# Optimization experiments

Hardware: AMD Instinct MI355X
Metric: run time of the kernel (lower is better)

The kernel has to match this reference:

```python
import jax, jax.numpy as jnp
import numpy as np

B, N, H, HEADS = 8, 1024, 512, 4  # batch graphs, nodes/graph, graph_hsz, attention heads
R = 64  # relations per graph (passthrough)


def setup_inputs() -> dict:
    key = jax.random.key(0)
    k1, k2, k3, k4, k5, k6, k7 = jax.random.split(key, 7)
    adjs = jax.random.randint(k1, (B, N, N), 0, 2, dtype=jnp.int32)  # 0 => masked
    nodes = jax.random.normal(k2, (B, N, H), dtype=jnp.float32)
    triples = jax.random.normal(k3, (B, R, H), dtype=jnp.float32)   # unused in gat path
    relations = jax.random.normal(k4, (B, R, H), dtype=jnp.float32)  # passthrough
    node_num = jnp.full((B,), N, dtype=jnp.int32)  # all graphs full => no padding branch
    s = 1.0 / np.sqrt(H)
    Wq = (jax.random.normal(k5, (H, H), dtype=jnp.float32) * s)
    Wk = (jax.random.normal(k6, (H, H), dtype=jnp.float32) * s)
    Wv = (jax.random.normal(k7, (H, H), dtype=jnp.float32) * s)
    return {"adjs": adjs, "triples": triples, "nodes": nodes, "node_num": node_num,
            "relations": relations, "Wq": Wq, "Wk": Wk, "Wv": Wv}


def reference(adjs, triples, nodes, node_num, relations, Wq, Wk, Wv):
    b, n, h = nodes.shape
    dk = h // HEADS
    scale = 1.0 / jnp.sqrt(jnp.float32(h))  # torch divides by sqrt(key_dim)=sqrt(H)

    def to_heads(x, W):  # [B,N,H] -> [B,heads,N,dk]; matches split(dim=-1)+stack
        return (x @ W).reshape(b, n, HEADS, dk).transpose(0, 2, 1, 3)

    Q = to_heads(nodes, Wq)
    K = to_heads(nodes, Wk)
    V = to_heads(nodes, Wv)
    att = jnp.einsum('bhnd,bhmd->bhnm', Q, K) * scale
    att = jnp.where((adjs == 0)[:, None, :, :], -jnp.inf, att)
    p = jax.nn.softmax(att, axis=-1)  # dropout_p = blockdrop = 0.0 => identity
    out = jnp.einsum('bhnm,bhmd->bhnd', p, V)
    out = out.transpose(0, 2, 1, 3).reshape(b, n, h)  # concat heads along feature dim
    out = jax.nn.relu(out)
    return (out, relations)
```

## Files before the change

### kernel.cpp

```cpp
#include <hip/hip_runtime.h>
#include <stdint.h>

typedef __attribute__((ext_vector_type(4))) float f32x4;
typedef __attribute__((ext_vector_type(8))) short bf16x8;
typedef unsigned long long ull;

#define GLB_AS const __attribute__((address_space(1)))
#define LDS_AS __attribute__((address_space(3)))

__device__ __forceinline__ short f2bf(float f) {
    union { float f; unsigned u; } x; x.f = f;
    unsigned r = x.u + 0x7FFFu + ((x.u >> 16) & 1u);
    return (short)(r >> 16);
}

__global__ void k_cvt_nodes(const float* __restrict__ in, short* __restrict__ out, int n) {
    int i = (blockIdx.x * 256 + threadIdx.x) * 8;
    if (i + 8 > n) return;
    float4 a = *(const float4*)(in + i);
    float4 b = *(const float4*)(in + i + 4);
    bf16x8 v;
    v[0] = f2bf(a.x); v[1] = f2bf(a.y); v[2] = f2bf(a.z); v[3] = f2bf(a.w);
    v[4] = f2bf(b.x); v[5] = f2bf(b.y); v[6] = f2bf(b.z); v[7] = f2bf(b.w);
    *(bf16x8*)(out + i) = v;
}

__global__ void k_cvt_wT(const float* __restrict__ Wq, const float* __restrict__ Wk,
                         const float* __restrict__ Wv, short* __restrict__ WT) {
    int g = blockIdx.x * 256 + threadIdx.x;
    int j = g >> 9;
    int k = g & 511;
    int w = j >> 9;
    int n = j & 511;
    const float* W = (w == 0) ? Wq : (w == 1) ? Wk : Wv;
    WT[g] = f2bf(W[k * 512 + n]);
}

__global__ void k_pack_adj(const int* __restrict__ adjs, unsigned* __restrict__ packed) {
    int g = blockIdx.x * 256 + threadIdx.x;
    int wv = g >> 6, lane = g & 63;
    ull m = __ballot(adjs[(size_t)wv * 64 + lane] != 0);
    if (lane == 0) *(ull*)(packed + (size_t)wv * 2) = m;
}

__global__ __launch_bounds__(256) void k_gemm_qkv(const short* __restrict__ A,
                                                  const short* __restrict__ WT,
                                                  short* __restrict__ C) {
    __shared__ short Asm[2][128 * 32];
    __shared__ short Bsm[2][128 * 32];
    const int tid = threadIdx.x;
    const int l = tid & 63, w = tid >> 6;
    const int wr = w >> 1, wc = w & 1;
    const int c16 = l & 15, g = l >> 4;
    const int row0 = blockIdx.x * 128, n0 = blockIdx.y * 128;
    f32x4 acc[4][4] = {};

    auto stage = [&](int kt, int bsel) {
        const int k0 = kt * 32;
#pragma unroll
        for (int i = 0; i < 2; ++i) {
            int ch = tid + 256 * i;
            int r = ch >> 2, gc = ch & 3;
            __builtin_amdgcn_global_load_lds((GLB_AS unsigned*)(A + (row0 + r) * 512 + k0 + 8 * gc),
                                             (LDS_AS unsigned*)(&Asm[bsel][ch * 8]), 16, 0, 0);
            __builtin_amdgcn_global_load_lds((GLB_AS unsigned*)(WT + (n0 + r) * 512 + k0 + 8 * gc),
                                             (LDS_AS unsigned*)(&Bsm[bsel][ch * 8]), 16, 0, 0);
        }
    };

    stage(0, 0);
    asm volatile("s_waitcnt vmcnt(0)" ::: "memory");
    __syncthreads();

    for (int kt = 0; kt < 16; ++kt) {
        const int cur = kt & 1;
        if (kt < 15) stage(kt + 1, cur ^ 1);
        bf16x8 af[4], bfr[4];
#pragma unroll
        for (int mf = 0; mf < 4; ++mf)
            af[mf] = *(const bf16x8*)&Asm[cur][(wr * 64 + mf * 16 + c16) * 32 + 8 * g];
#pragma unroll
        for (int nf = 0; nf < 4; ++nf)
            bfr[nf] = *(const bf16x8*)&Bsm[cur][(wc * 64 + nf * 16 + c16) * 32 + 8 * g];
#pragma unroll
        for (int mf = 0; mf < 4; ++mf)
#pragma unroll
            for (int nf = 0; nf < 4; ++nf)
                acc[mf][nf] = __builtin_amdgcn_mfma_f32_16x16x32_bf16(af[mf], bfr[nf], acc[mf][nf], 0, 0, 0);
        asm volatile("s_waitcnt vmcnt(0)" ::: "memory");
        __syncthreads();
    }
#pragma unroll
    for (int mf = 0; mf < 4; ++mf)
#pragma unroll
        for (int nf = 0; nf < 4; ++nf)
#pragma unroll
            for (int r = 0; r < 4; ++r) {
                int row = row0 + wr * 64 + mf * 16 + 4 * g + r;
                int col = n0 + wc * 64 + nf * 16 + c16;
                C[row * 1536 + col] = f2bf(acc[mf][nf][r]);
            }
}

__global__ __launch_bounds__(256) void k_transpose_v(const short* __restrict__ QKV, short* __restrict__ Vt) {
    __shared__ short tile[64 * 65];
    const int b = blockIdx.x, n0 = blockIdx.y * 64, d0 = blockIdx.z * 64;
    const int t = threadIdx.x;
#pragma unroll
    for (int i = 0; i < 16; ++i) {
        int idx = t + 256 * i;
        int nn = idx >> 6, dd = idx & 63;
        tile[nn * 65 + dd] = QKV[(b * 1024 + n0 + nn) * 1536 + 1024 + d0 + dd];
    }
    __syncthreads();
#pragma unroll
    for (int i = 0; i < 16; ++i) {
        int idx = t + 256 * i;
        int dd = idx >> 6, nn = idx & 63;
        Vt[(b * 512 + d0 + dd) * 1024 + n0 + nn] = tile[nn * 65 + dd];
    }
}

__global__ __launch_bounds__(256) void k_attn(const short* __restrict__ QKV, const short* __restrict__ Vt,
                                              const unsigned* __restrict__ packed, float* __restrict__ out) {
    __shared__ short Ksm[2][64 * 128];
    __shared__ short Vsm[2][128 * 64];
    __shared__ short Psm[64 * 72];
    const int bh = blockIdx.x;
    const int b = bh >> 2, h = bh & 3;
    const int q0 = blockIdx.y * 64;
    const int tid = threadIdx.x, l = tid & 63, w = tid >> 6;
    const int c16 = l & 15, g = l >> 4;
    const int qw = q0 + w * 16;
    const float scale = 0.044194173824159216f;

    bf16x8 aq[4];
    const short* Qrow = QKV + (size_t)(b * 1024 + qw + c16) * 1536 + h * 128;
#pragma unroll
    for (int kf = 0; kf < 4; ++kf)
        aq[kf] = *(const bf16x8*)(Qrow + kf * 32 + 8 * g);

    f32x4 acc_o[8] = {};
    float l_lane[4] = {0.f, 0.f, 0.f, 0.f};

    const short* Kbase = QKV + (size_t)(b * 1024) * 1536 + 512 + h * 128;
    const short* Vtbase = Vt + (size_t)(b * 512 + h * 128) * 1024;
    const ull* adjp = (const ull*)packed + (size_t)(b * 1024 + qw + 4 * g) * 16;

    auto stage = [&](int t, int bsel) {
        const int m0 = t * 64;
#pragma unroll
        for (int i = 0; i < 4; ++i) {
            int ch = tid + 256 * i;
            int mr = ch >> 4, gc = ch & 15;
            int gs = gc ^ (mr & 7);
            __builtin_amdgcn_global_load_lds((GLB_AS unsigned*)(Kbase + (size_t)(m0 + mr) * 1536 + 8 * gs),
                                             (LDS_AS unsigned*)(&Ksm[bsel][ch * 8]), 16, 0, 0);
        }
#pragma unroll
        for (int i = 0; i < 4; ++i) {
            int ch = tid + 256 * i;
            int dr = ch >> 3, gc = ch & 7;
            int gs = gc ^ (dr & 7);
            __builtin_amdgcn_global_load_lds((GLB_AS unsigned*)(Vtbase + (size_t)dr * 1024 + m0 + 8 * gs),
                                             (LDS_AS unsigned*)(&Vsm[bsel][ch * 8]), 16, 0, 0);
        }
    };

    ull mcur[4], mnxt[4] = {0, 0, 0, 0};
    stage(0, 0);
#pragma unroll
    for (int r = 0; r < 4; ++r) mcur[r] = adjp[r * 16];
    asm volatile("s_waitcnt vmcnt(0)" ::: "memory");
    __syncthreads();

    for (int t = 0; t < 16; ++t) {
        const int cur = t & 1;
        if (t < 15) {
            stage(t + 1, cur ^ 1);
#pragma unroll
            for (int r = 0; r < 4; ++r) mnxt[r] = adjp[r * 16 + t + 1];
        }

        f32x4 s[4] = {};
#pragma unroll
        for (int nf = 0; nf < 4; ++nf) {
            const int mrow = nf * 16 + c16;
#pragma unroll
            for (int kf = 0; kf < 4; ++kf) {
                int chunk = (kf * 4 + g) ^ (mrow & 7);
                bf16x8 bk = *(const bf16x8*)&Ksm[cur][mrow * 128 + chunk * 8];
                s[nf] = __builtin_amdgcn_mfma_f32_16x16x32_bf16(aq[kf], bk, s[nf], 0, 0, 0);
            }
        }
#pragma unroll
        for (int r = 0; r < 4; ++r) {
            unsigned mlo = (unsigned)mcur[r];
            unsigned mhi = (unsigned)(mcur[r] >> 32);
#pragma unroll
            for (int nf = 0; nf < 4; ++nf) {
                unsigned hw = (nf < 2) ? mlo : mhi;
                unsigned bit = (hw >> ((nf & 1) * 16 + c16)) & 1u;
                float e = __expf(s[nf][r] * scale);
                float pv = bit ? e : 0.f;
                l_lane[r] += pv;
                Psm[(w * 16 + 4 * g + r) * 72 + nf * 16 + c16] = f2bf(pv);
            }
        }
#pragma unroll
        for (int ks = 0; ks < 2; ++ks) {
            bf16x8 ap = *(const bf16x8*)&Psm[(w * 16 + c16) * 72 + ks * 32 + 8 * g];
#pragma unroll
            for (int df = 0; df < 8; ++df) {
                const int drow = df * 16 + c16;
                int chunk = (ks * 4 + g) ^ (drow & 7);
                bf16x8 bv = *(const bf16x8*)&Vsm[cur][drow * 64 + chunk * 8];
                acc_o[df] = __builtin_amdgcn_mfma_f32_16x16x32_bf16(ap, bv, acc_o[df], 0, 0, 0);
            }
        }
        asm volatile("s_waitcnt vmcnt(0)" ::: "memory");
        __syncthreads();
#pragma unroll
        for (int r = 0; r < 4; ++r) mcur[r] = mnxt[r];
    }
    float inv_l[4];
#pragma unroll
    for (int r = 0; r < 4; ++r) {
        float ls = l_lane[r];
        ls += __shfl_xor(ls, 1);
        ls += __shfl_xor(ls, 2);
        ls += __shfl_xor(ls, 4);
        ls += __shfl_xor(ls, 8);
        inv_l[r] = 1.f / ls;
    }
#pragma unroll
    for (int df = 0; df < 8; ++df)
#pragma unroll
        for (int r = 0; r < 4; ++r) {
            int q = qw + 4 * g + r;
            float o = fmaxf(acc_o[df][r] * inv_l[r], 0.f);
            out[(size_t)(b * 1024 + q) * 512 + h * 128 + df * 16 + c16] = o;
        }
}

__global__ void k_copy_rel(const float* __restrict__ in, float* __restrict__ out, int n) {
    int i = (blockIdx.x * 256 + threadIdx.x) * 4;
    if (i + 4 > n) return;
    *(float4*)(out + i) = *(const float4*)(in + i);
}

extern "C" void kernel_launch(void* const* d_in, const int* in_sizes, int n_in,
                              void* d_out, int out_size, void* d_ws, size_t ws_size,
                              hipStream_t stream) {
    const int*   adjs      = (const int*)d_in[0];
    const float* nodes     = (const float*)d_in[2];
    const float* relations = (const float*)d_in[4];
    const float* Wq        = (const float*)d_in[5];
    const float* Wk        = (const float*)d_in[6];
    const float* Wv        = (const float*)d_in[7];

    char* ws = (char*)d_ws;
    short* nodes_bf   = (short*)(ws);
    short* WT         = (short*)(ws + 8388608);
    short* QKV        = (short*)(ws + 9961472);
    short* Vt         = (short*)(ws + 35127296);
    unsigned* adjpack = (unsigned*)(ws + 43515904);

    float* out     = (float*)d_out;
    float* out_rel = out + 4194304;

    k_cvt_nodes<<<dim3(2048), dim3(256), 0, stream>>>(nodes, nodes_bf, 4194304);
    k_cvt_wT<<<dim3(3072), dim3(256), 0, stream>>>(Wq, Wk, Wv, WT);
    k_pack_adj<<<dim3(32768), dim3(256), 0, stream>>>(adjs, adjpack);
    k_gemm_qkv<<<dim3(64, 12), dim3(256), 0, stream>>>(nodes_bf, WT, QKV);
    k_transpose_v<<<dim3(8, 16, 8), dim3(256), 0, stream>>>(QKV, Vt);
    k_attn<<<dim3(32, 16), dim3(256), 0, stream>>>(QKV, Vt, adjpack, out);
    k_copy_rel<<<dim3(256), dim3(256), 0, stream>>>(relations, out_rel, 262144);
}
```

Measured before the change: 91.63 us.

## Merge preprocessing kernels, swizzle GEMM tiles, and restructure attention softmax pipeline

Folds the three preprocessing kernels into one launch and the relation copy into the V-transpose launch, cutting the launch count from seven to four. Remaps GEMM workgroups with an XCD-aware swizzle to improve cache locality. In attention, computes S transposed so each lane holds four consecutive key columns. It uses exp2 with a prescaled constant, packed bf16 conversion and per-wave P buffers. It also replaces full syncthreads with partial vmcnt waits plus raw barriers and sets wave priority around the MFMA blocks. The finer-grained waits risk ordering bugs if the vmcnt counts are wrong.

```diff
diff --git a/kernel.cpp b/kernel.cpp
--- a/kernel.cpp
+++ b/kernel.cpp
@@ -14,33 +14,31 @@
     return (short)(r >> 16);
 }
 
-__global__ void k_cvt_nodes(const float* __restrict__ in, short* __restrict__ out, int n) {
-    int i = (blockIdx.x * 256 + threadIdx.x) * 8;
-    if (i + 8 > n) return;
-    float4 a = *(const float4*)(in + i);
-    float4 b = *(const float4*)(in + i + 4);
-    bf16x8 v;
-    v[0] = f2bf(a.x); v[1] = f2bf(a.y); v[2] = f2bf(a.z); v[3] = f2bf(a.w);
-    v[4] = f2bf(b.x); v[5] = f2bf(b.y); v[6] = f2bf(b.z); v[7] = f2bf(b.w);
-    *(bf16x8*)(out + i) = v;
-}
-
-__global__ void k_cvt_wT(const float* __restrict__ Wq, const float* __restrict__ Wk,
-                         const float* __restrict__ Wv, short* __restrict__ WT) {
-    int g = blockIdx.x * 256 + threadIdx.x;
-    int j = g >> 9;
-    int k = g & 511;
-    int w = j >> 9;
-    int n = j & 511;
-    const float* W = (w == 0) ? Wq : (w == 1) ? Wk : Wv;
-    WT[g] = f2bf(W[k * 512 + n]);
-}
-
-__global__ void k_pack_adj(const int* __restrict__ adjs, unsigned* __restrict__ packed) {
-    int g = blockIdx.x * 256 + threadIdx.x;
-    int wv = g >> 6, lane = g & 63;
-    ull m = __ballot(adjs[(size_t)wv * 64 + lane] != 0);
-    if (lane == 0) *(ull*)(packed + (size_t)wv * 2) = m;
+__global__ void k_pre(const float* __restrict__ nodes, short* __restrict__ nodes_bf,
+                      const float* __restrict__ Wq, const float* __restrict__ Wk,
+                      const float* __restrict__ Wv, short* __restrict__ WT,
+                      const int* __restrict__ adjs, unsigned* __restrict__ packed) {
+    int bi = blockIdx.x, tid = threadIdx.x;
+    if (bi < 2048) {
+        int i = (bi * 256 + tid) * 8;
+        float4 a = *(const float4*)(nodes + i);
+        float4 b = *(const float4*)(nodes + i + 4);
+        bf16x8 v;
+        v[0] = f2bf(a.x); v[1] = f2bf(a.y); v[2] = f2bf(a.z); v[3] = f2bf(a.w);
+        v[4] = f2bf(b.x); v[5] = f2bf(b.y); v[6] = f2bf(b.z); v[7] = f2bf(b.w);
+        *(bf16x8*)(nodes_bf + i) = v;
+    } else if (bi < 5120) {
+        int g = (bi - 2048) * 256 + tid;
+        int j = g >> 9, k = g & 511;
+        int w = j >> 9, n = j & 511;
+        const float* W = (w == 0) ? Wq : (w == 1) ? Wk : Wv;
+        WT[g] = f2bf(W[k * 512 + n]);
+    } else {
+        int g = (bi - 5120) * 256 + tid;
+        int wv = g >> 6, lane = g & 63;
+        ull m = __ballot(adjs[(size_t)wv * 64 + lane] != 0);
+        if (lane == 0) *(ull*)(packed + (size_t)wv * 2) = m;
+    }
 }
 
 __global__ __launch_bounds__(256) void k_gemm_qkv(const short* __restrict__ A,
@@ -52,7 +50,9 @@
     const int l = tid & 63, w = tid >> 6;
     const int wr = w >> 1, wc = w & 1;
     const int c16 = l & 15, g = l >> 4;
-    const int row0 = blockIdx.x * 128, n0 = blockIdx.y * 128;
+    const int wg = blockIdx.x;
+    const int swz = (wg & 7) * 96 + (wg >> 3);
+    const int row0 = (swz / 12) * 128, n0 = (swz % 12) * 128;
     f32x4 acc[4][4] = {};
 
     auto stage = [&](int kt, int bsel) {
@@ -102,10 +102,16 @@
             }
 }
 
-__global__ __launch_bounds__(256) void k_transpose_v(const short* __restrict__ QKV, short* __restrict__ Vt) {
+__global__ __launch_bounds__(256) void k_mid(const short* __restrict__ QKV, short* __restrict__ Vt,
+                                             const float* __restrict__ rel_in, float* __restrict__ rel_out) {
     __shared__ short tile[64 * 65];
-    const int b = blockIdx.x, n0 = blockIdx.y * 64, d0 = blockIdx.z * 64;
-    const int t = threadIdx.x;
+    const int bi = blockIdx.x, t = threadIdx.x;
+    if (bi >= 1024) {
+        int i = ((bi - 1024) * 256 + t) * 4;
+        *(float4*)(rel_out + i) = *(const float4*)(rel_in + i);
+        return;
+    }
+    const int b = bi >> 7, n0 = ((bi >> 3) & 15) * 64, d0 = (bi & 7) * 64;
 #pragma unroll
     for (int i = 0; i < 16; ++i) {
         int idx = t + 256 * i;
@@ -125,14 +131,14 @@
                                               const unsigned* __restrict__ packed, float* __restrict__ out) {
     __shared__ short Ksm[2][64 * 128];
     __shared__ short Vsm[2][128 * 64];
-    __shared__ short Psm[64 * 72];
+    __shared__ short Psm[4][16 * 68];
     const int bh = blockIdx.x;
     const int b = bh >> 2, h = bh & 3;
     const int q0 = blockIdx.y * 64;
-    const int tid = threadIdx.x, l = tid & 63, w = tid >> 6;
+    const int tid = threadIdx.x, l = tid & 63, wid = tid >> 6;
     const int c16 = l & 15, g = l >> 4;
-    const int qw = q0 + w * 16;
-    const float scale = 0.044194173824159216f;
+    const int qw = q0 + wid * 16;
+    const float kscale = 0.06375872022286384f;
 
     bf16x8 aq[4];
     const short* Qrow = QKV + (size_t)(b * 1024 + qw + c16) * 1536 + h * 128;
@@ -141,11 +147,11 @@
         aq[kf] = *(const bf16x8*)(Qrow + kf * 32 + 8 * g);
 
     f32x4 acc_o[8] = {};
-    float l_lane[4] = {0.f, 0.f, 0.f, 0.f};
+    float l_lane = 0.f;
 
     const short* Kbase = QKV + (size_t)(b * 1024) * 1536 + 512 + h * 128;
     const short* Vtbase = Vt + (size_t)(b * 512 + h * 128) * 1024;
-    const ull* adjp = (const ull*)packed + (size_t)(b * 1024 + qw + 4 * g) * 16;
+    const ull* adjq = (const ull*)packed + (size_t)(b * 1024 + qw + c16) * 16;
 
     auto stage = [&](int t, int bsel) {
         const int m0 = t * 64;
@@ -167,72 +173,85 @@
         }
     };
 
-    ull mcur[4], mnxt[4] = {0, 0, 0, 0};
+    ull mcur, mnxt = 0;
+    mcur = adjq[0];
     stage(0, 0);
-#pragma unroll
-    for (int r = 0; r < 4; ++r) mcur[r] = adjp[r * 16];
     asm volatile("s_waitcnt vmcnt(0)" ::: "memory");
-    __syncthreads();
+    __builtin_amdgcn_s_barrier();
 
     for (int t = 0; t < 16; ++t) {
         const int cur = t & 1;
         if (t < 15) {
+            mnxt = adjq[t + 1];
             stage(t + 1, cur ^ 1);
-#pragma unroll
-            for (int r = 0; r < 4; ++r) mnxt[r] = adjp[r * 16 + t + 1];
         }
 
         f32x4 s[4] = {};
+        __builtin_amdgcn_s_setprio(1);
 #pragma unroll
         for (int nf = 0; nf < 4; ++nf) {
             const int mrow = nf * 16 + c16;
 #pragma unroll
             for (int kf = 0; kf < 4; ++kf) {
                 int chunk = (kf * 4 + g) ^ (mrow & 7);
-                bf16x8 bk = *(const bf16x8*)&Ksm[cur][mrow * 128 + chunk * 8];
-                s[nf] = __builtin_amdgcn_mfma_f32_16x16x32_bf16(aq[kf], bk, s[nf], 0, 0, 0);
+                bf16x8 ak = *(const bf16x8*)&Ksm[cur][mrow * 128 + chunk * 8];
+                s[nf] = __builtin_amdgcn_mfma_f32_16x16x32_bf16(ak, aq[kf], s[nf], 0, 0, 0);
             }
         }
-#pragma unroll
-        for (int r = 0; r < 4; ++r) {
-            unsigned mlo = (unsigned)mcur[r];
-            unsigned mhi = (unsigned)(mcur[r] >> 32);
-#pragma unroll
-            for (int nf = 0; nf < 4; ++nf) {
-                unsigned hw = (nf < 2) ? mlo : mhi;
-                unsigned bit = (hw >> ((nf & 1) * 16 + c16)) & 1u;
-                float e = __expf(s[nf][r] * scale);
-                float pv = bit ? e : 0.f;
-                l_lane[r] += pv;
-                Psm[(w * 16 + 4 * g + r) * 72 + nf * 16 + c16] = f2bf(pv);
-            }
-        }
+        __builtin_amdgcn_s_setprio(0);
+
+        unsigned mlo = (unsigned)mcur, mhi = (unsigned)(mcur >> 32);
+#pragma unroll
+        for (int nf = 0; nf < 4; ++nf) {
+            unsigned hw = (nf < 2) ? mlo : mhi;
+            unsigned nib = (hw >> ((nf & 1) * 16 + 4 * g)) & 15u;
+            float p0 = (nib & 1u) ? __builtin_amdgcn_exp2f(s[nf][0] * kscale) : 0.f;
+            float p1 = (nib & 2u) ? __builtin_amdgcn_exp2f(s[nf][1] * kscale) : 0.f;
+            float p2 = (nib & 4u) ? __builtin_amdgcn_exp2f(s[nf][2] * kscale) : 0.f;
+            float p3 = (nib & 8u) ? __builtin_amdgcn_exp2f(s[nf][3] * kscale) : 0.f;
+            l_lane += (p0 + p1) + (p2 + p3);
+            unsigned lo, hi;
+            asm("v_cvt_pk_bf16_f32 %0, %1, %2" : "=v"(lo) : "v"(p0), "v"(p1));
+            asm("v_cvt_pk_bf16_f32 %0, %1, %2" : "=v"(hi) : "v"(p2), "v"(p3));
+            ull wv = ((ull)hi << 32) | lo;
+            *(ull*)&Psm[wid][c16 * 68 + nf * 16 + 4 * g] = wv;
+        }
+
+        if (t < 15) { asm volatile("s_waitcnt vmcnt(9)" ::: "memory"); }
+        else        { asm volatile("s_waitcnt vmcnt(0)" ::: "memory"); }
+        __builtin_amdgcn_s_barrier();
+
+        __builtin_amdgcn_s_setprio(1);
 #pragma unroll
         for (int ks = 0; ks < 2; ++ks) {
-            bf16x8 ap = *(const bf16x8*)&Psm[(w * 16 + c16) * 72 + ks * 32 + 8 * g];
+            union { ull u[2]; bf16x8 v; } ap;
+            ap.u[0] = *(const ull*)&Psm[wid][c16 * 68 + ks * 32 + 8 * g];
+            ap.u[1] = *(const ull*)&Psm[wid][c16 * 68 + ks * 32 + 8 * g + 4];
 #pragma unroll
             for (int df = 0; df < 8; ++df) {
                 const int drow = df * 16 + c16;
                 int chunk = (ks * 4 + g) ^ (drow & 7);
                 bf16x8 bv = *(const bf16x8*)&Vsm[cur][drow * 64 + chunk * 8];
-                acc_o[df] = __builtin_amdgcn_mfma_f32_16x16x32_bf16(ap, bv, acc_o[df], 0, 0, 0);
+                acc_o[df] = __builtin_amdgcn_mfma_f32_16x16x32_bf16(ap.v, bv, acc_o[df], 0, 0, 0);
             }
         }
-        asm volatile("s_waitcnt vmcnt(0)" ::: "memory");
-        __syncthreads();
-#pragma unroll
-        for (int r = 0; r < 4; ++r) mcur[r] = mnxt[r];
-    }
+        __builtin_amdgcn_s_setprio(0);
+
+        mcur = mnxt;
+
+        if (t < 15) {
+            asm volatile("s_waitcnt vmcnt(4)" ::: "memory");
+            __builtin_amdgcn_s_barrier();
+        }
+    }
+
+    l_lane += __shfl_xor(l_lane, 16);
+    l_lane += __shfl_xor(l_lane, 32);
     float inv_l[4];
 #pragma unroll
-    for (int r = 0; r < 4; ++r) {
-        float ls = l_lane[r];
-        ls += __shfl_xor(ls, 1);
-        ls += __shfl_xor(ls, 2);
-        ls += __shfl_xor(ls, 4);
-        ls += __shfl_xor(ls, 8);
-        inv_l[r] = 1.f / ls;
-    }
+    for (int r = 0; r < 4; ++r)
+        inv_l[r] = 1.f / __shfl(l_lane, 4 * g + r);
+
 #pragma unroll
     for (int df = 0; df < 8; ++df)
 #pragma unroll
@@ -241,12 +260,6 @@
             float o = fmaxf(acc_o[df][r] * inv_l[r], 0.f);
             out[(size_t)(b * 1024 + q) * 512 + h * 128 + df * 16 + c16] = o;
         }
-}
-
-__global__ void k_copy_rel(const float* __restrict__ in, float* __restrict__ out, int n) {
-    int i = (blockIdx.x * 256 + threadIdx.x) * 4;
-    if (i + 4 > n) return;
-    *(float4*)(out + i) = *(const float4*)(in + i);
 }
 
 extern "C" void kernel_launch(void* const* d_in, const int* in_sizes, int n_in,
@@ -269,11 +282,8 @@
     float* out     = (float*)d_out;
     float* out_rel = out + 4194304;
 
-    k_cvt_nodes<<<dim3(2048), dim3(256), 0, stream>>>(nodes, nodes_bf, 4194304);
-    k_cvt_wT<<<dim3(3072), dim3(256), 0, stream>>>(Wq, Wk, Wv, WT);
-    k_pack_adj<<<dim3(32768), dim3(256), 0, stream>>>(adjs, adjpack);
-    k_gemm_qkv<<<dim3(64, 12), dim3(256), 0, stream>>>(nodes_bf, WT, QKV);
-    k_transpose_v<<<dim3(8, 16, 8), dim3(256), 0, stream>>>(QKV, Vt);
+    k_pre<<<dim3(37888), dim3(256), 0, stream>>>(nodes, nodes_bf, Wq, Wk, Wv, WT, adjs, adjpack);
+    k_gemm_qkv<<<dim3(768), dim3(256), 0, stream>>>(nodes_bf, WT, QKV);
+    k_mid<<<dim3(1280), dim3(256), 0, stream>>>(QKV, Vt, relations, out_rel);
     k_attn<<<dim3(32, 16), dim3(256), 0, stream>>>(QKV, Vt, adjpack, out);
-    k_copy_rel<<<dim3(256), dim3(256), 0, stream>>>(relations, out_rel, 262144);
-}
+}
```

Measured after the change: 81.21 us. 1.13x faster.
